# Kernel tuning notes

Measured on AMD Instinct MI355X. Metric: run time of the kernel, lower is better.

Reference implementation:

```python
import math
import jax, jax.numpy as jnp
import numpy as np

F_MUL = 48   # multiplicity of node irreps: 48x0e + 48x1o + 48x2e
K = 16       # num_keep
P = 2        # num_poles
B = 8        # number of graphs in the batch


def _su2_cg(j1, j2, j3, m1, m2, m3):
    if m1 + m2 != m3:
        return 0.0
    f = math.factorial
    pre = ((2 * j3 + 1) * f(j3 + j1 - j2) * f(j3 - j1 + j2) * f(j1 + j2 - j3) / f(j1 + j2 + j3 + 1)) ** 0.5
    pre *= (f(j3 + m3) * f(j3 - m3) * f(j1 - m1) * f(j1 + m1) * f(j2 - m2) * f(j2 + m2)) ** 0.5
    s = 0.0
    for v in range(0, j1 + j2 - j3 + 1):
        args = [v, j1 + j2 - j3 - v, j1 - m1 - v, j2 + m2 - v, j3 - j2 + m1 + v, j3 - j1 - m2 + v]
        if min(args) < 0:
            continue
        den = 1
        for a in args:
            den *= f(a)
        s += (-1) ** v / den
    return pre * s


def _u_c2r(l):
    # complex -> real spherical-harmonics change of basis
    U = np.zeros((2 * l + 1, 2 * l + 1), dtype=complex)
    s2 = 2 ** -0.5
    for m in range(-l, l + 1):
        a = l + m
        if m > 0:
            U[a, l + m] = (-1) ** m * s2
            U[a, l - m] = s2
        elif m == 0:
            U[a, l] = 1.0
        else:
            U[a, l + m] = 1j * s2
            U[a, l - m] = -1j * (-1) ** m * s2
    return U


def _real_cg(l1, l2, l3):
    Cc = np.zeros((2 * l1 + 1, 2 * l2 + 1, 2 * l3 + 1), dtype=complex)
    for a, m1 in enumerate(range(-l1, l1 + 1)):
        for b, m2 in enumerate(range(-l2, l2 + 1)):
            for c, m3 in enumerate(range(-l3, l3 + 1)):
                Cc[a, b, c] = _su2_cg(l1, l2, l3, m1, m2, m3)
    U1, U2, U3 = _u_c2r(l1), _u_c2r(l2), _u_c2r(l3)
    C = np.einsum('ap,bq,cr,pqr->abc', np.conj(U1), np.conj(U2), U3, Cc)
    C = C.imag if np.abs(C.imag).max() > np.abs(C.real).max() else C.real
    nrm = np.linalg.norm(C)
    return np.asarray(C / max(nrm, 1e-12), dtype=np.float32)  # unit Frobenius norm (e3nn w3j convention)

# uvu tensor-product paths (l1, l2, l3): node x node -> {0e,1o,2e}
PATHS = [(0, 0, 0), (0, 1, 1), (0, 2, 2), (1, 0, 1), (1, 1, 0), (1, 1, 2), (1, 2, 1), (2, 0, 2), (2, 1, 1), (2, 2, 0), (2, 2, 2)]
CG = {lls: jnp.asarray(_real_cg(*lls)) for lls in set(PATHS) | {(1, 1, 2)}}


def setup_inputs() -> dict:
    key = jax.random.key(0)
    ks = jax.random.split(key, 12)
    n, Fm = 512, F_MUL
    return {
        'node_feats': jax.random.normal(ks[0], (n, 9 * Fm), jnp.float32),
        'W_lin0': jax.random.normal(ks[1], (Fm, Fm), jnp.float32),
        'W_lin1': jax.random.normal(ks[2], (Fm, Fm), jnp.float32),
        'W_lin2': jax.random.normal(ks[3], (Fm, Fm), jnp.float32),
        'tp_w': jax.random.normal(ks[4], (len(PATHS), Fm, Fm), jnp.float32),
        'W_out0': jax.random.normal(ks[5], (3 * Fm, K * Fm), jnp.float32),
        'W_out1': jax.random.normal(ks[6], (4 * Fm, K * Fm), jnp.float32),
        'W_out2': jax.random.normal(ks[7], (4 * Fm, K * Fm), jnp.float32),
        'Wt0': jax.random.normal(ks[8], (K, 2), jnp.float32),
        'Wt1': jax.random.normal(ks[9], (K, 1), jnp.float32),
        'Wt2': jax.random.normal(ks[10], (K, 1), jnp.float32),
        'batch': jnp.sort(jax.random.randint(ks[11], (n,), 0, B)),
        'max_nodes': 128,
    }


def reference(node_feats, W_lin0, W_lin1, W_lin2, tp_w, W_out0, W_out1, W_out2, Wt0, Wt1, Wt2, batch, max_nodes):
    n = node_feats.shape[0]
    Fm = F_MUL
    # split into l=0,1,2 blocks: [n, F, 2l+1]
    x = [node_feats[:, :Fm].reshape(n, Fm, 1),
         node_feats[:, Fm:4 * Fm].reshape(n, Fm, 3),
         node_feats[:, 4 * Fm:9 * Fm].reshape(n, Fm, 5)]
    sF = np.float32(Fm) ** -0.5
    # linear_diag: per-l channel mixing
    y = [jnp.einsum('nui,uv->nvi', xl, W) * sF for xl, W in zip(x, (W_lin0, W_lin1, W_lin2))]
    # conv_tp_diag: uvu tensor product of y with itself, one slot per path
    outs = {0: [], 1: [], 2: []}
    for p, (l1, l2, l3) in enumerate(PATHS):
        a = jnp.einsum('nvk,uv->nuk', y[l2], tp_w[p]) * sF
        outs[l3].append(jnp.einsum('num,nuk,mkc->nuc', y[l1], a, CG[(l1, l2, l3)]))
    h = []
    for l, Wo in ((0, W_out0), (1, W_out1), (2, W_out2)):
        o = jnp.concatenate(outs[l], axis=1)  # [n, n_paths*F, 2l+1]
        h.append(jnp.einsum('nui,uv->nvi', o, Wo) * np.float32(o.shape[1]) ** -0.5)  # [n, K*F, 2l+1]
    # reshape_irreps: [n, K*F, 2l+1] -> [n, F, K, 2l+1]
    r = [hl.reshape(n, K, Fm, 2 * l + 1).transpose(0, 2, 1, 3) for l, hl in enumerate(h)]
    sK = np.float32(K) ** -0.5
    g0 = jnp.einsum('nfki,ko->nfoi', r[0], Wt0) * sK  # [n,F,2,1]
    g1 = jnp.einsum('nfki,ko->nfoi', r[1], Wt1) * sK  # [n,F,1,3]
    g2 = jnp.einsum('nfki,ko->nfoi', r[2], Wt2) * sK  # [n,F,1,5]
    a0, a1 = g0[:, :, 0, 0], g0[:, :, 1, 0]
    v, d = g1[:, :, 0, :], g2[:, :, 0, :]
    # symmetric 4x4 block per (node, feature): [[a0, v], [v, a1*I/sqrt3 + CG(1,1,2).d]]
    S = a1[..., None, None] * (jnp.eye(3, dtype=a1.dtype) * np.float32(3) ** -0.5) \
        + jnp.einsum('nfm,ijm->nfij', d, CG[(1, 1, 2)])
    top = jnp.concatenate([a0[..., None, None], v[:, :, None, :]], axis=-1)  # [n,F,1,4]
    bot = jnp.concatenate([v[..., None], S], axis=-1)                        # [n,F,3,4]
    M = jnp.concatenate([top, bot], axis=2)                                  # [n,F,4,4]
    D = 4 * Fm
    big = jnp.einsum('nfij,fg->nfigj', M, jnp.eye(Fm, dtype=M.dtype)).reshape(n, D, D)
    H = jnp.broadcast_to(big[:, None], (n, P, D, D))  # repeat over poles
    # to_dense_batch
    counts = jax.ops.segment_sum(jnp.ones((n,), jnp.int32), batch, num_segments=B)
    starts = jnp.concatenate([jnp.zeros((1,), jnp.int32), jnp.cumsum(counts)[:-1]])
    pos = jnp.arange(n) - starts[batch]
    return jnp.zeros((B, max_nodes, P, D, D), H.dtype).at[batch, pos].set(H, mode='drop')
```

## Files before the change

### kernel.cpp

```cpp
#include <hip/hip_runtime.h>


__device__ const int ZOFF[11] = {0,48,192,432,480,624,768,1008,1056,1200,1440};
__device__ const int NOFF[11] = {0,48,192,432,576,624,864,1008,1248,1392,1440};
__device__ const int OOFF[11] = {0,144,720,288,48,960,432,1200,576,96,1440};
__device__ const int PL2[11]  = {0,1,2,0,1,1,2,0,1,2,2};
__device__ const int PL3[11]  = {0,1,2,1,0,2,1,2,1,0,2};

#define R10f 0.31622776601683794f
#define R30f 0.18257418583505536f
#define A70f 0.23904572186687872f
#define B70f 0.11952286093343936f
#define T70f 0.20701966780270626f

__device__ const float CG112[3][3][5] = {
  {{0,0,-R30f,0,-R10f},{0,R10f,0,0,0},{R10f,0,0,0,0}},
  {{0,R10f,0,0,0},{0,0,2.0f*R30f,0,0},{0,0,0,R10f,0}},
  {{R10f,0,0,0,0},{0,0,0,R10f,0},{0,0,-R30f,0,R10f}}
};

__device__ const float CG121[3][5][3] = {
  {{0,0,-R10f},{0,-R10f,0},{R30f,0,0},{0,0,0},{R10f,0,0}},
  {{0,0,0},{-R10f,0,0},{0,-2.0f*R30f,0},{0,0,-R10f},{0,0,0}},
  {{-R10f,0,0},{0,0,0},{0,0,R30f},{0,-R10f,0},{0,0,-R10f}}
};

__device__ const float CG222[5][5][5] = {
  {{0,0,A70f,0,0},{0,0,0,-T70f,0},{A70f,0,0,0,0},{0,-T70f,0,0,0},{0,0,0,0,0}},
  {{0,0,0,-T70f,0},{0,0,-B70f,0,T70f},{0,-B70f,0,0,0},{-T70f,0,0,0,0},{0,T70f,0,0,0}},
  {{A70f,0,0,0,0},{0,-B70f,0,0,0},{0,0,-A70f,0,0},{0,0,0,-B70f,0},{0,0,0,0,A70f}},
  {{0,-T70f,0,0,0},{-T70f,0,0,0,0},{0,0,0,-B70f,0},{0,0,-B70f,0,-T70f},{0,0,0,-T70f,0}},
  {{0,0,0,0,0},{0,T70f,0,0,0},{0,0,0,0,A70f},{0,0,0,-T70f,0},{0,0,A70f,0,0}}
};

__global__ void weff_kernel(const float* __restrict__ Wo0, const float* __restrict__ Wo1,
                            const float* __restrict__ Wo2, const float* __restrict__ Wt0,
                            const float* __restrict__ Wt1, const float* __restrict__ Wt2,
                            float* __restrict__ weff0, float* __restrict__ weff1,
                            float* __restrict__ weff2) {
  int idx = blockIdx.x * 256 + threadIdx.x;
  const float s0  = 1.0f / 48.0f;
  const float s12 = 0.018042195912175807f;
  if (idx < 13824) {
    int u = idx % 144, fo = idx / 144;
    int f = fo >> 1, o = fo & 1;
    float acc = 0.0f;
    for (int k = 0; k < 16; ++k) acc += Wo0[u*768 + k*48 + f] * Wt0[k*2 + o];
    weff0[idx] = acc * s0;
  } else if (idx < 23040) {
    int j = idx - 13824; int u = j % 192, f = j / 192;
    float acc = 0.0f;
    for (int k = 0; k < 16; ++k) acc += Wo1[u*768 + k*48 + f] * Wt1[k];
    weff1[j] = acc * s12;
  } else if (idx < 32256) {
    int j = idx - 23040; int u = j % 192, f = j / 192;
    float acc = 0.0f;
    for (int k = 0; k < 16; ++k) acc += Wo2[u*768 + k*48 + f] * Wt2[k];
    weff2[j] = acc * s12;
  }
}

__global__ void starts_kernel(const int* __restrict__ batch, int n, int* __restrict__ starts) {
  int b = threadIdx.x;
  if (b < 9) {
    int c = 0;
    for (int i = 0; i < n; ++i) c += (batch[i] < b) ? 1 : 0;
    starts[b] = c;
  }
}

__global__ __launch_bounds__(256) void node_kernel(
    const float* __restrict__ feats, const float* __restrict__ Wl0,
    const float* __restrict__ Wl1, const float* __restrict__ Wl2,
    const float* __restrict__ tpw, const float* __restrict__ weff0,
    const float* __restrict__ weff1, const float* __restrict__ weff2,
    float* __restrict__ mblk) {
  const int node = blockIdx.x;
  const int tid = threadIdx.x;
  const float sF = 0.14433756729740643f;

  __shared__ float xs[432];
  __shared__ float ys[432];
  __shared__ float zs[1680];
  __shared__ float os[1680];
  __shared__ float gs[480];

  const float* fr = feats + node * 432;
  for (int t = tid; t < 432; t += 256) xs[t] = fr[t];
  __syncthreads();

  for (int t = tid; t < 432; t += 256) {
    float acc = 0.0f;
    if (t < 48) {
      int v = t;
      for (int u = 0; u < 48; ++u) acc += xs[u] * Wl0[u*48 + v];
    } else if (t < 192) {
      int j = t - 48, v = j / 3, i = j % 3;
      for (int u = 0; u < 48; ++u) acc += xs[48 + u*3 + i] * Wl1[u*48 + v];
    } else {
      int j = t - 192, v = j / 5, i = j % 5;
      for (int u = 0; u < 48; ++u) acc += xs[192 + u*5 + i] * Wl2[u*48 + v];
    }
    ys[t] = acc * sF;
  }
  __syncthreads();

  for (int t = tid; t < 1680; t += 256) {
    int p = 10; while (ZOFF[p] > t) --p;
    int j = t - ZOFF[p];
    int l2 = PL2[p], K2 = 2*l2 + 1;
    int u = j / K2, k = j % K2;
    const float* tw = tpw + p*2304 + u*48;
    const float* yy = ys + (l2 == 0 ? 0 : (l2 == 1 ? 48 : 192));
    float acc = 0.0f;
    for (int v = 0; v < 48; ++v) acc += tw[v] * yy[v*K2 + k];
    zs[t] = acc * sF;
  }
  __syncthreads();

  for (int t = tid; t < 1680; t += 256) {
    int p = 10; while (NOFF[p] > t) --p;
    int j = t - NOFF[p];
    int K3 = 2*PL3[p] + 1;
    int u = j / K3, c = j % K3;
    const float* zp = zs + ZOFF[p];
    float acc = 0.0f;
    switch (p) {
      case 0: acc = ys[u] * zp[u]; break;
      case 1: acc = 0.5773502691896258f * ys[u] * zp[u*3 + c]; break;
      case 2: acc = 0.4472135954999579f * ys[u] * zp[u*5 + c]; break;
      case 3: acc = 0.5773502691896258f * ys[48 + u*3 + c] * zp[u]; break;
      case 4: { float s = 0.0f;
                for (int m = 0; m < 3; ++m) s += ys[48 + u*3 + m] * zp[u*3 + m];
                acc = -0.5773502691896258f * s; } break;
      case 5: for (int m = 0; m < 3; ++m)
                for (int k = 0; k < 3; ++k)
                  acc += ys[48 + u*3 + m] * zp[u*3 + k] * CG112[m][k][c];
              break;
      case 6: for (int m = 0; m < 3; ++m)
                for (int k = 0; k < 5; ++k)
                  acc += ys[48 + u*3 + m] * zp[u*5 + k] * CG121[m][k][c];
              break;
      case 7: acc = 0.4472135954999579f * ys[192 + u*5 + c] * zp[u]; break;
      case 8: for (int m = 0; m < 5; ++m)
                for (int k = 0; k < 3; ++k)
                  acc += ys[192 + u*5 + m] * zp[u*3 + k] * CG121[k][m][c];
              break;
      case 9: { float s = 0.0f;
                for (int m = 0; m < 5; ++m) s += ys[192 + u*5 + m] * zp[u*5 + m];
                acc = 0.4472135954999579f * s; } break;
      default: for (int m = 0; m < 5; ++m)
                 for (int k = 0; k < 5; ++k)
                   acc += ys[192 + u*5 + m] * zp[u*5 + k] * CG222[m][k][c];
               break;
    }
    os[OOFF[p] + u*K3 + c] = acc;
  }
  __syncthreads();

  for (int t = tid; t < 480; t += 256) {
    float acc = 0.0f;
    if (t < 96) {
      const float* w = weff0 + t * 144;
      for (int u = 0; u < 144; ++u) acc += os[u] * w[u];
    } else if (t < 240) {
      int j = t - 96, f = j / 3, i = j % 3;
      const float* w = weff1 + f * 192;
      for (int u = 0; u < 192; ++u) acc += os[144 + u*3 + i] * w[u];
    } else {
      int j = t - 240, f = j / 5, m = j % 5;
      const float* w = weff2 + f * 192;
      for (int u = 0; u < 192; ++u) acc += os[720 + u*5 + m] * w[u];
    }
    gs[t] = acc;
  }
  __syncthreads();

  if (tid < 192) {
    int f = tid >> 2, i = tid & 3;
    float a0 = gs[f*2 + 0], a1 = gs[f*2 + 1];
    float v0 = gs[96 + f*3 + 0], v1 = gs[96 + f*3 + 1], v2 = gs[96 + f*3 + 2];
    float d0 = gs[240 + f*5 + 0], d1 = gs[240 + f*5 + 1], d2 = gs[240 + f*5 + 2];
    float d3 = gs[240 + f*5 + 3], d4 = gs[240 + f*5 + 4];
    const float R3i = 0.5773502691896258f;
    float m0, m1, m2, m3;
    if (i == 0)      { m0 = a0; m1 = v0; m2 = v1; m3 = v2; }
    else if (i == 1) { m0 = v0; m1 = a1*R3i - R30f*d2 - R10f*d4; m2 = R10f*d1; m3 = R10f*d0; }
    else if (i == 2) { m0 = v1; m1 = R10f*d1; m2 = a1*R3i + 2.0f*R30f*d2; m3 = R10f*d3; }
    else             { m0 = v2; m1 = R10f*d0; m2 = R10f*d3; m3 = a1*R3i - R30f*d2 + R10f*d4; }
    *(float4*)(mblk + node * 768 + (tid << 2)) = make_float4(m0, m1, m2, m3);
  }
}

__global__ __launch_bounds__(256) void fill_kernel(const float* __restrict__ mblk,
                                                   const int* __restrict__ starts,
                                                   float* __restrict__ out) {
  const int tid = threadIdx.x;
  const int b = blockIdx.z, pos = blockIdx.y;
  const int s0 = starts[b], s1 = starts[b + 1];
  const int node = s0 + pos;
  const bool valid = node < s1;
  float* dst = out + (size_t)(b * gridDim.y + pos) * 73728u;
  const float4 zero = make_float4(0.f, 0.f, 0.f, 0.f);
  const int base = blockIdx.x * 2048 + tid;
  #pragma unroll
  for (int k = 0; k < 8; ++k) {
    int idx = base + k * 256;
    int j = idx % 48;
    int row = (idx / 48) % 192;
    float4 val = zero;
    if (valid && j == (row >> 2)) {
      val = *(const float4*)(mblk + node * 768 + (row << 2));
    }
    *(float4*)(dst + (size_t)idx * 4) = val;
  }
}

extern "C" void kernel_launch(void* const* d_in, const int* in_sizes, int n_in,
                              void* d_out, int out_size, void* d_ws, size_t ws_size,
                              hipStream_t stream) {
  const float* feats = (const float*)d_in[0];
  const float* Wl0   = (const float*)d_in[1];
  const float* Wl1   = (const float*)d_in[2];
  const float* Wl2   = (const float*)d_in[3];
  const float* tpw   = (const float*)d_in[4];
  const float* Wo0   = (const float*)d_in[5];
  const float* Wo1   = (const float*)d_in[6];
  const float* Wo2   = (const float*)d_in[7];
  const float* Wt0   = (const float*)d_in[8];
  const float* Wt1   = (const float*)d_in[9];
  const float* Wt2   = (const float*)d_in[10];
  const int*   batch = (const int*)d_in[11];

  int n = in_sizes[0] / 432;
  int max_nodes = out_size / (8 * 2 * 192 * 192);

  float* ws     = (float*)d_ws;
  float* weff0  = ws;
  float* weff1  = ws + 13824;
  float* weff2  = ws + 23040;
  int*   starts = (int*)(ws + 32256);
  float* mblk   = ws + 32272;

  weff_kernel<<<126, 256, 0, stream>>>(Wo0, Wo1, Wo2, Wt0, Wt1, Wt2, weff0, weff1, weff2);
  starts_kernel<<<1, 64, 0, stream>>>(batch, n, starts);
  node_kernel<<<n, 256, 0, stream>>>(feats, Wl0, Wl1, Wl2, tpw, weff0, weff1, weff2, mblk);
  fill_kernel<<<dim3(9, max_nodes, 8), 256, 0, stream>>>(mblk, starts, (float*)d_out);
}
```

Baseline: 412.7 us.

## Merge prep kernels, unroll inner loops, use nontemporal stores in fill

Folds the starts computation into the weight-folding kernel as an extra block, which saves one launch. Adds unroll pragmas to the node kernel's small reduction loops. Switches the fill kernel's large zero-padded output writes to nontemporal vector stores so the streaming output bypasses the cache. The fill kernel writes a large dense output and likely dominates runtime, so the store change is the main lever.

```diff
diff --git a/kernel.cpp b/kernel.cpp
--- a/kernel.cpp
+++ b/kernel.cpp
@@ -1,5 +1,7 @@
 #include <hip/hip_runtime.h>
 
+
+typedef float f32x4 __attribute__((ext_vector_type(4)));
 
 __device__ const int ZOFF[11] = {0,48,192,432,480,624,768,1008,1056,1200,1440};
 __device__ const int NOFF[11] = {0,48,192,432,576,624,864,1008,1248,1392,1440};
@@ -33,11 +35,13 @@
   {{0,0,0,0,0},{0,T70f,0,0,0},{0,0,0,0,A70f},{0,0,0,-T70f,0},{0,0,A70f,0,0}}
 };
 
-__global__ void weff_kernel(const float* __restrict__ Wo0, const float* __restrict__ Wo1,
-                            const float* __restrict__ Wo2, const float* __restrict__ Wt0,
-                            const float* __restrict__ Wt1, const float* __restrict__ Wt2,
-                            float* __restrict__ weff0, float* __restrict__ weff1,
-                            float* __restrict__ weff2) {
+__global__ __launch_bounds__(256) void prep_kernel(
+    const float* __restrict__ Wo0, const float* __restrict__ Wo1,
+    const float* __restrict__ Wo2, const float* __restrict__ Wt0,
+    const float* __restrict__ Wt1, const float* __restrict__ Wt2,
+    const int* __restrict__ batch, int n,
+    float* __restrict__ weff0, float* __restrict__ weff1,
+    float* __restrict__ weff2, int* __restrict__ starts) {
   int idx = blockIdx.x * 256 + threadIdx.x;
   const float s0  = 1.0f / 48.0f;
   const float s12 = 0.018042195912175807f;
@@ -45,25 +49,23 @@
     int u = idx % 144, fo = idx / 144;
     int f = fo >> 1, o = fo & 1;
     float acc = 0.0f;
+    #pragma unroll
     for (int k = 0; k < 16; ++k) acc += Wo0[u*768 + k*48 + f] * Wt0[k*2 + o];
     weff0[idx] = acc * s0;
   } else if (idx < 23040) {
     int j = idx - 13824; int u = j % 192, f = j / 192;
     float acc = 0.0f;
+    #pragma unroll
     for (int k = 0; k < 16; ++k) acc += Wo1[u*768 + k*48 + f] * Wt1[k];
     weff1[j] = acc * s12;
   } else if (idx < 32256) {
     int j = idx - 23040; int u = j % 192, f = j / 192;
     float acc = 0.0f;
+    #pragma unroll
     for (int k = 0; k < 16; ++k) acc += Wo2[u*768 + k*48 + f] * Wt2[k];
     weff2[j] = acc * s12;
-  }
-}
-
-__global__ void starts_kernel(const int* __restrict__ batch, int n, int* __restrict__ starts) {
-  int b = threadIdx.x;
-  if (b < 9) {
-    int c = 0;
+  } else if (blockIdx.x == 126 && threadIdx.x < 9) {
+    int b = threadIdx.x, c = 0;
     for (int i = 0; i < n; ++i) c += (batch[i] < b) ? 1 : 0;
     starts[b] = c;
   }
@@ -93,12 +95,15 @@
     float acc = 0.0f;
     if (t < 48) {
       int v = t;
+      #pragma unroll
       for (int u = 0; u < 48; ++u) acc += xs[u] * Wl0[u*48 + v];
     } else if (t < 192) {
       int j = t - 48, v = j / 3, i = j % 3;
+      #pragma unroll
       for (int u = 0; u < 48; ++u) acc += xs[48 + u*3 + i] * Wl1[u*48 + v];
     } else {
       int j = t - 192, v = j / 5, i = j % 5;
+      #pragma unroll
       for (int u = 0; u < 48; ++u) acc += xs[192 + u*5 + i] * Wl2[u*48 + v];
     }
     ys[t] = acc * sF;
@@ -113,6 +118,7 @@
     const float* tw = tpw + p*2304 + u*48;
     const float* yy = ys + (l2 == 0 ? 0 : (l2 == 1 ? 48 : 192));
     float acc = 0.0f;
+    #pragma unroll
     for (int v = 0; v < 48; ++v) acc += tw[v] * yy[v*K2 + k];
     zs[t] = acc * sF;
   }
@@ -131,28 +137,46 @@
       case 2: acc = 0.4472135954999579f * ys[u] * zp[u*5 + c]; break;
       case 3: acc = 0.5773502691896258f * ys[48 + u*3 + c] * zp[u]; break;
       case 4: { float s = 0.0f;
+                #pragma unroll
                 for (int m = 0; m < 3; ++m) s += ys[48 + u*3 + m] * zp[u*3 + m];
                 acc = -0.5773502691896258f * s; } break;
-      case 5: for (int m = 0; m < 3; ++m)
-                for (int k = 0; k < 3; ++k)
-                  acc += ys[48 + u*3 + m] * zp[u*3 + k] * CG112[m][k][c];
-              break;
-      case 6: for (int m = 0; m < 3; ++m)
-                for (int k = 0; k < 5; ++k)
-                  acc += ys[48 + u*3 + m] * zp[u*5 + k] * CG121[m][k][c];
-              break;
+      case 5: {
+                #pragma unroll
+                for (int m = 0; m < 3; ++m) {
+                  #pragma unroll
+                  for (int k = 0; k < 3; ++k)
+                    acc += ys[48 + u*3 + m] * zp[u*3 + k] * CG112[m][k][c];
+                }
+              } break;
+      case 6: {
+                #pragma unroll
+                for (int m = 0; m < 3; ++m) {
+                  #pragma unroll
+                  for (int k = 0; k < 5; ++k)
+                    acc += ys[48 + u*3 + m] * zp[u*5 + k] * CG121[m][k][c];
+                }
+              } break;
       case 7: acc = 0.4472135954999579f * ys[192 + u*5 + c] * zp[u]; break;
-      case 8: for (int m = 0; m < 5; ++m)
-                for (int k = 0; k < 3; ++k)
-                  acc += ys[192 + u*5 + m] * zp[u*3 + k] * CG121[k][m][c];
-              break;
+      case 8: {
+                #pragma unroll
+                for (int m = 0; m < 5; ++m) {
+                  #pragma unroll
+                  for (int k = 0; k < 3; ++k)
+                    acc += ys[192 + u*5 + m] * zp[u*3 + k] * CG121[k][m][c];
+                }
+              } break;
       case 9: { float s = 0.0f;
+                #pragma unroll
                 for (int m = 0; m < 5; ++m) s += ys[192 + u*5 + m] * zp[u*5 + m];
                 acc = 0.4472135954999579f * s; } break;
-      default: for (int m = 0; m < 5; ++m)
-                 for (int k = 0; k < 5; ++k)
-                   acc += ys[192 + u*5 + m] * zp[u*5 + k] * CG222[m][k][c];
-               break;
+      default: {
+                #pragma unroll
+                for (int m = 0; m < 5; ++m) {
+                  #pragma unroll
+                  for (int k = 0; k < 5; ++k)
+                    acc += ys[192 + u*5 + m] * zp[u*5 + k] * CG222[m][k][c];
+                }
+              } break;
     }
     os[OOFF[p] + u*K3 + c] = acc;
   }
@@ -162,14 +186,17 @@
     float acc = 0.0f;
     if (t < 96) {
       const float* w = weff0 + t * 144;
+      #pragma unroll 4
       for (int u = 0; u < 144; ++u) acc += os[u] * w[u];
     } else if (t < 240) {
       int j = t - 96, f = j / 3, i = j % 3;
       const float* w = weff1 + f * 192;
+      #pragma unroll 4
       for (int u = 0; u < 192; ++u) acc += os[144 + u*3 + i] * w[u];
     } else {
       int j = t - 240, f = j / 5, m = j % 5;
       const float* w = weff2 + f * 192;
+      #pragma unroll 4
       for (int u = 0; u < 192; ++u) acc += os[720 + u*5 + m] * w[u];
     }
     gs[t] = acc;
@@ -201,18 +228,17 @@
   const int node = s0 + pos;
   const bool valid = node < s1;
   float* dst = out + (size_t)(b * gridDim.y + pos) * 73728u;
-  const float4 zero = make_float4(0.f, 0.f, 0.f, 0.f);
   const int base = blockIdx.x * 2048 + tid;
   #pragma unroll
   for (int k = 0; k < 8; ++k) {
     int idx = base + k * 256;
     int j = idx % 48;
     int row = (idx / 48) % 192;
-    float4 val = zero;
+    f32x4 val = (f32x4)0.0f;
     if (valid && j == (row >> 2)) {
-      val = *(const float4*)(mblk + node * 768 + (row << 2));
-    }
-    *(float4*)(dst + (size_t)idx * 4) = val;
+      val = *(const f32x4*)(mblk + node * 768 + (row << 2));
+    }
+    __builtin_nontemporal_store(val, (f32x4*)(dst + (size_t)idx * 4));
   }
 }
 
@@ -242,8 +268,8 @@
   int*   starts = (int*)(ws + 32256);
   float* mblk   = ws + 32272;
 
-  weff_kernel<<<126, 256, 0, stream>>>(Wo0, Wo1, Wo2, Wt0, Wt1, Wt2, weff0, weff1, weff2);
-  starts_kernel<<<1, 64, 0, stream>>>(batch, n, starts);
+  prep_kernel<<<127, 256, 0, stream>>>(Wo0, Wo1, Wo2, Wt0, Wt1, Wt2, batch, n,
+                                       weff0, weff1, weff2, starts);
   node_kernel<<<n, 256, 0, stream>>>(feats, Wl0, Wl1, Wl2, tpw, weff0, weff1, weff2, mblk);
   fill_kernel<<<dim3(9, max_nodes, 8), 256, 0, stream>>>(mblk, starts, (float*)d_out);
 }
```

Result: no change. 407.5 us (-1.3%).
